# Kernel tuning notes

Hardware: AMD Instinct MI355X
Metric: run time of the kernel (lower is better)

## Reference

```python
import jax, jax.numpy as jnp
import numpy as np

# ---- constants mirroring the torch module ----
LOSS_ALPHA = 1.0      # args.loss_weight_alpha (intra-class weight)
LOSS_BETA = 1.0       # args.loss_weight_beta (focal weight)
FOCAL_GAMMA = 2.0
FOCAL_ALPHA = 0.85
EPS = 1e-09
LDAM_S = 30.0
CLS_NUM = np.array([85.0, 900.0])
LDAM_MAX_M = 0.5
LDAM_W = np.array([0.15, 0.85], dtype=np.float32)
B = 16777216


def setup_inputs() -> dict:
    key = jax.random.key(0)
    k1, k2 = jax.random.split(key)
    x = jax.random.uniform(k1, (B, 2), dtype=jnp.float32)  # [B, 2] probabilities-like logits
    target = jax.random.randint(k2, (B,), 0, 2)            # binary labels
    return {"x": x, "target": target}


def _intraclass_p(centered, std, target, cls):
    # correlation between consecutive same-class rows (sorted-index order),
    # vectorized: class-c indices first via stable argsort, mask invalid pairs.
    n_rows = centered.shape[0]
    mask = target == cls
    n = jnp.sum(mask)
    order = jnp.argsort(jnp.where(mask, jnp.arange(n_rows), n_rows))
    a, b = order[:-1], order[1:]
    corr = jnp.sum(centered[a] * centered[b], axis=1) / (std[a] * std[b])
    valid = jnp.arange(n_rows - 1) < (n - 1)
    s = jnp.sum(jnp.where(valid, corr, 0.0))
    return jnp.where(n > 0, s / jnp.maximum(n, 1).astype(s.dtype), 0.0)


def reference(x, target):
    num_cls = x.shape[1]
    # ---- LDAM loss ----
    m = 1.0 / np.sqrt(np.sqrt(CLS_NUM))
    m = m * (LDAM_MAX_M / np.max(m))
    m_list = jnp.asarray(m, jnp.float32)
    w = jnp.asarray(LDAM_W)
    batch_m = m_list[target]                                      # [B]
    onehot = jax.nn.one_hot(target, num_cls, dtype=bool)          # [B, C]
    out = jnp.where(onehot, x - batch_m[:, None], x)              # margin on target logit only
    logsm = jax.nn.log_softmax(LDAM_S * out, axis=-1)
    nll = -jnp.take_along_axis(logsm, target[:, None], axis=1)[:, 0]
    wi = w[target]
    ldam = jnp.sum(wi * nll) / jnp.sum(wi)                        # weighted-mean cross entropy
    # ---- binary focal loss (treats x[:,1] as probability) ----
    p = x[:, 1]
    t = target.astype(x.dtype)
    fl = (-FOCAL_ALPHA * t * (1.0 - p) ** FOCAL_GAMMA * jnp.log(p + EPS)
          - (1.0 - FOCAL_ALPHA) * (1.0 - t) * p ** FOCAL_GAMMA * jnp.log(1.0 - p + EPS))
    focal = jnp.mean(fl)
    # ---- intra-class correlation loss ----
    centered = x - jnp.mean(x, axis=1, keepdims=True)
    std = jnp.std(x, axis=1, ddof=1)                               # torch.std default: unbiased
    p0 = _intraclass_p(centered, std, target, 0)
    p1 = _intraclass_p(centered, std, target, 1)
    intra = (p0 - p1) ** 2
    return ldam + LOSS_BETA * focal + LOSS_ALPHA * intra
```

## Files before the change

kernel.cpp:

```cpp
#include <hip/hip_runtime.h>

#define E_BLOCK 8192
#define E_WAVE  2048
#define ITERS   16

#define M1      0.2771814156f
#define LDAM_S  30.0f

struct BlockRec {
  int s0, p0, s1, p1;
  float wnll, fl;
  int cnt1, pad;
};

__device__ __forceinline__ void comb0(int &s, int &f, int &l, int sb, int fb, int lb) {
  s += sb + l * fb;
  f = f ? f : fb;
  l = fb ? lb : l;
}

__device__ __forceinline__ void bfly_step(int m, int lane, int &s, int &f, int &l) {
  const int os = __shfl_xor(s, m), of = __shfl_xor(f, m), ol = __shfl_xor(l, m);
  const bool up = (lane & m) != 0;
  int as = up ? os : s, af = up ? of : f, al = up ? ol : l;
  const int bs = up ? s : os, bf = up ? f : of, bl = up ? l : ol;
  comb0(as, af, al, bs, bf, bl);
  s = as; f = af; l = al;
}

__global__ __launch_bounds__(256) void loss_pass1(
    const float* __restrict__ x, const int* __restrict__ tgt,
    BlockRec* __restrict__ recs, int B) {
  __shared__ unsigned int lds[3328];
  unsigned int* chunkw = lds;
  unsigned int* stw = lds + 2304;
  float* wnw = (float*)(lds + 2560);
  float* flw = (float*)(lds + 2816);
  int*   cnw = (int*)(lds + 3072);
  unsigned short* cs = (unsigned short*)lds;

  const int tid = threadIdx.x;
  const int w = tid >> 6, lane = tid & 63;
  const int waveBase = blockIdx.x * E_BLOCK + w * E_WAVE;

  float wnll = 0.f, fls = 0.f; int cnt1 = 0;

  for (int j = 0; j < ITERS; ++j) {
    const int e = waveBase + ((j << 6) + lane) * 2;
    unsigned int pk = 0;
    if (e < B) {
      const float4 xv = *reinterpret_cast<const float4*>(x + 2 * e);
      const int2  tv = *reinterpret_cast<const int2*>(tgt + e);
      unsigned int c[2];
      const float x0a = xv.x, x1a = xv.y; const float x0b = xv.z, x1b = xv.w;
      const int ta = tv.x, tb = tv.y;
      {
        const float d  = x0a - x1a;
        const float z  = LDAM_S * (ta ? (d + M1) : (0.5f - d));
        const float sp = fmaxf(z, 0.f) + __logf(1.f + __expf(-fabsf(z)));
        wnll += (ta ? 0.85f : 0.15f) * sp;
        const float p  = x1a;
        const float lg = __logf((ta ? p : (1.f - p)) + 1e-9f);
        const float cf = ta ? (-0.85f * (1.f - p) * (1.f - p)) : (-0.15f * p * p);
        fls += cf * lg;
        cnt1 += ta;
        c[0] = 4u | (unsigned)(x0a > x1a) | ((unsigned)ta << 1);
      }
      {
        const float d  = x0b - x1b;
        const float z  = LDAM_S * (tb ? (d + M1) : (0.5f - d));
        const float sp = fmaxf(z, 0.f) + __logf(1.f + __expf(-fabsf(z)));
        wnll += (tb ? 0.85f : 0.15f) * sp;
        const float p  = x1b;
        const float lg = __logf((tb ? p : (1.f - p)) + 1e-9f);
        const float cf = tb ? (-0.85f * (1.f - p) * (1.f - p)) : (-0.15f * p * p);
        fls += cf * lg;
        cnt1 += tb;
        c[1] = 4u | (unsigned)(x0b > x1b) | ((unsigned)tb << 1);
      }
      pk = c[0] | (c[1] << 8);
    }
    const int li2 = w * 1024 + (j << 6) + lane;
    cs[(li2 >> 4) * 18 + (li2 & 15)] = (unsigned short)pk;
  }
  __syncthreads();

  int s0 = 0, f0 = 0, l0 = 0, s1 = 0, f1 = 0, l1 = 0;
  #pragma unroll
  for (int r = 0; r < 8; ++r) {
    const unsigned int wv = chunkw[tid * 9 + r];
    #pragma unroll
    for (int k = 0; k < 4; ++k) {
      const unsigned int b = (wv >> (8 * k)) & 7u;
      if (b & 4u) {
        const int sv = (int)((b & 1u) << 1) - 1;
        const int t  = (int)((b >> 1) & 1u);
        const int lv = t ? l1 : l0;
        const int add = lv * sv;
        if (t) { s1 += add; l1 = sv; f1 = f1 ? f1 : sv; }
        else   { s0 += add; l0 = sv; f0 = f0 ? f0 : sv; }
      }
    }
  }
  stw[tid] = (unsigned)(s0 + 128) | ((unsigned)(f0 + 1) << 8) | ((unsigned)(l0 + 1) << 10)
           | ((unsigned)(s1 + 128) << 16) | ((unsigned)(f1 + 1) << 24) | ((unsigned)(l1 + 1) << 26);
  wnw[tid] = wnll; flw[tid] = fls; cnw[tid] = cnt1;
  __syncthreads();

  if (w == 0) {
    int S0 = 0, F0 = 0, L0 = 0, S1 = 0, F1 = 0, L1 = 0;
    float W = 0.f, F = 0.f; int C = 0;
    #pragma unroll
    for (int q = 0; q < 4; ++q) {
      const int i = lane * 4 + q;
      const unsigned int pk = stw[i];
      comb0(S0, F0, L0, (int)(pk & 255u) - 128, (int)((pk >> 8) & 3u) - 1, (int)((pk >> 10) & 3u) - 1);
      comb0(S1, F1, L1, (int)((pk >> 16) & 255u) - 128, (int)((pk >> 24) & 3u) - 1, (int)((pk >> 26) & 3u) - 1);
      W += wnw[i]; F += flw[i]; C += cnw[i];
    }
    #pragma unroll
    for (int k = 0; k < 6; ++k) {
      const int m = 1 << k;
      bfly_step(m, lane, S0, F0, L0);
      bfly_step(m, lane, S1, F1, L1);
      W += __shfl_xor(W, m); F += __shfl_xor(F, m); C += __shfl_xor(C, m);
    }
    if (lane == 0) {
      BlockRec r;
      r.s0 = S0; r.p0 = (F0 + 1) | ((L0 + 1) << 4);
      r.s1 = S1; r.p1 = (F1 + 1) | ((L1 + 1) << 4);
      r.wnll = W; r.fl = F; r.cnt1 = C; r.pad = 0;
      recs[blockIdx.x] = r;
    }
  }
}

__global__ __launch_bounds__(256) void loss_pass2(
    const BlockRec* __restrict__ recs, int NB, int B, float* __restrict__ out) {
  __shared__ int sS0[256], sF0[256], sL0[256], sS1[256], sF1[256], sL1[256], sC[256];
  __shared__ double sW[256], sFl[256];
  const int tid = threadIdx.x, w = tid >> 6, lane = tid & 63;
  const int R = (NB + 255) >> 8;

  int s0 = 0, f0 = 0, l0 = 0, s1 = 0, f1 = 0, l1 = 0;
  double W = 0.0, Fd = 0.0; int C = 0;
  for (int r = 0; r < R; ++r) {
    const int b = tid * R + r;
    if (b < NB) {
      const BlockRec rec = recs[b];
      comb0(s0, f0, l0, rec.s0, (rec.p0 & 3) - 1, ((rec.p0 >> 4) & 3) - 1);
      comb0(s1, f1, l1, rec.s1, (rec.p1 & 3) - 1, ((rec.p1 >> 4) & 3) - 1);
      W += (double)rec.wnll; Fd += (double)rec.fl; C += rec.cnt1;
    }
  }
  sS0[tid] = s0; sF0[tid] = f0; sL0[tid] = l0;
  sS1[tid] = s1; sF1[tid] = f1; sL1[tid] = l1;
  sC[tid] = C; sW[tid] = W; sFl[tid] = Fd;
  __syncthreads();

  if (w == 0) {
    int S0 = 0, F0 = 0, L0 = 0, S1 = 0, F1 = 0, L1 = 0; int Ct = 0;
    double Wt = 0.0, Ft = 0.0;
    #pragma unroll
    for (int q = 0; q < 4; ++q) {
      const int i = lane * 4 + q;
      comb0(S0, F0, L0, sS0[i], sF0[i], sL0[i]);
      comb0(S1, F1, L1, sS1[i], sF1[i], sL1[i]);
      Wt += sW[i]; Ft += sFl[i]; Ct += sC[i];
    }
    #pragma unroll
    for (int k = 0; k < 6; ++k) {
      const int m = 1 << k;
      bfly_step(m, lane, S0, F0, L0);
      bfly_step(m, lane, S1, F1, L1);
      Wt += __shfl_xor(Wt, m); Ft += __shfl_xor(Ft, m); Ct += __shfl_xor(Ct, m);
    }
    if (lane == 0) {
      const double n1 = (double)Ct, n0 = (double)B - n1;
      const double sw = 0.15 * n0 + 0.85 * n1;
      const double ldam  = Wt / sw;
      const double focal = Ft / (double)B;
      const double q0 = (n0 > 0.0) ? (double)S0 / n0 : 0.0;
      const double q1 = (n1 > 0.0) ? (double)S1 / n1 : 0.0;
      const double dq = q0 - q1;
      out[0] = (float)(ldam + focal + dq * dq);
    }
  }
}

extern "C" void kernel_launch(void* const* d_in, const int* in_sizes, int n_in,
                              void* d_out, int out_size, void* d_ws, size_t ws_size,
                              hipStream_t stream) {
  const float* x  = (const float*)d_in[0];
  const int* tgt  = (const int*)d_in[1];
  float* out      = (float*)d_out;
  const int B  = in_sizes[1];
  const int NB = (B + E_BLOCK - 1) / E_BLOCK;
  BlockRec* recs = (BlockRec*)d_ws;
  loss_pass1<<<NB, 256, 0, stream>>>(x, tgt, recs, B);
  loss_pass2<<<1, 256, 0, stream>>>(recs, NB, B, out);
}
```

Measured before the change: 245.0 us.

## Process four elements per lane with prefetched loads and branchless exp2/log2 math

Each lane now handles four consecutive elements per iteration using two float4 loads and one int4 target load. The next iteration's data is prefetched into registers before the current one is computed. The per-element math becomes branchless FMA form using the hardware exp2/log2 builtins, the ln2 scaling of the focal term is folded into one multiply at the end, and packed sign codes are written to shared memory as 32-bit words. A launch bound of 8 blocks per CU is added, which may constrain register allocation, and a separate scalar tail path covers partial waves.

```diff
diff --git a/kernel.cpp b/kernel.cpp
--- a/kernel.cpp
+++ b/kernel.cpp
@@ -2,10 +2,14 @@
 
 #define E_BLOCK 8192
 #define E_WAVE  2048
-#define ITERS   16
-
-#define M1      0.2771814156f
-#define LDAM_S  30.0f
+#define QITERS  8
+
+#define M1f     0.2771814156f
+#define C_A1    60.0f
+#define C_C1    (30.0f*M1f - 15.0f)
+
+#define EXP2F(v) __builtin_amdgcn_exp2f(v)
+#define LOG2F(v) __builtin_amdgcn_logf(v)
 
 struct BlockRec {
   int s0, p0, s1, p1;
@@ -28,7 +32,31 @@
   s = as; f = af; l = al;
 }
 
-__global__ __launch_bounds__(256) void loss_pass1(
+__device__ __forceinline__ void elem_math(float x0, float x1, int t, int k,
+                                          float &wnll, float &flraw, int &cnt1,
+                                          unsigned int &word) {
+  const float tf  = (float)t;
+  const float wgt = fmaf(tf, 0.7f, 0.15f);
+  const float d   = x0 - x1;
+  const float za  = fmaf(tf, C_A1, -30.0f);
+  const float zc  = fmaf(tf, C_C1, 15.0f);
+  const float z   = fmaf(za, d, zc);
+  const float ex  = EXP2F(fabsf(z) * -1.44269504f);
+  const float lp  = LOG2F(1.0f + ex);
+  const float sp  = fmaf(0.69314718f, lp, fmaxf(z, 0.0f));
+  wnll = fmaf(wgt, sp, wnll);
+  const float om  = 1.0f - x1;
+  const float q   = t ? x1 : om;
+  const float r   = t ? om : x1;
+  const float lg2 = LOG2F(q + 1e-9f);
+  const float wr2 = (wgt * r) * r;
+  flraw = fmaf(wr2, lg2, flraw);
+  cnt1 += t;
+  const unsigned int code = 4u | (unsigned int)(d > 0.0f) | ((unsigned int)t << 1);
+  word |= code << (8 * k);
+}
+
+__global__ __launch_bounds__(256, 8) void loss_pass1(
     const float* __restrict__ x, const int* __restrict__ tgt,
     BlockRec* __restrict__ recs, int B) {
   __shared__ unsigned int lds[3328];
@@ -37,51 +65,48 @@
   float* wnw = (float*)(lds + 2560);
   float* flw = (float*)(lds + 2816);
   int*   cnw = (int*)(lds + 3072);
-  unsigned short* cs = (unsigned short*)lds;
 
   const int tid = threadIdx.x;
   const int w = tid >> 6, lane = tid & 63;
   const int waveBase = blockIdx.x * E_BLOCK + w * E_WAVE;
 
-  float wnll = 0.f, fls = 0.f; int cnt1 = 0;
-
-  for (int j = 0; j < ITERS; ++j) {
-    const int e = waveBase + ((j << 6) + lane) * 2;
-    unsigned int pk = 0;
-    if (e < B) {
-      const float4 xv = *reinterpret_cast<const float4*>(x + 2 * e);
-      const int2  tv = *reinterpret_cast<const int2*>(tgt + e);
-      unsigned int c[2];
-      const float x0a = xv.x, x1a = xv.y; const float x0b = xv.z, x1b = xv.w;
-      const int ta = tv.x, tb = tv.y;
-      {
-        const float d  = x0a - x1a;
-        const float z  = LDAM_S * (ta ? (d + M1) : (0.5f - d));
-        const float sp = fmaxf(z, 0.f) + __logf(1.f + __expf(-fabsf(z)));
-        wnll += (ta ? 0.85f : 0.15f) * sp;
-        const float p  = x1a;
-        const float lg = __logf((ta ? p : (1.f - p)) + 1e-9f);
-        const float cf = ta ? (-0.85f * (1.f - p) * (1.f - p)) : (-0.15f * p * p);
-        fls += cf * lg;
-        cnt1 += ta;
-        c[0] = 4u | (unsigned)(x0a > x1a) | ((unsigned)ta << 1);
+  float wnll = 0.f, flraw = 0.f; int cnt1 = 0;
+
+  if (waveBase + E_WAVE <= B) {
+    const int e0 = waveBase + lane * 4;
+    const float4* __restrict__ px = (const float4*)(x + 2 * (size_t)e0);
+    const int4*   __restrict__ pt = (const int4*)(tgt + e0);
+
+    float4 xa = px[0], xb = px[1];
+    int4  t4 = pt[0];
+    for (int j = 0; j < QITERS; ++j) {
+      float4 xa_n, xb_n; int4 t4_n;
+      if (j + 1 < QITERS) {
+        const int o = (j + 1) * 128;
+        xa_n = px[o]; xb_n = px[o + 1]; t4_n = pt[(j + 1) * 64];
       }
-      {
-        const float d  = x0b - x1b;
-        const float z  = LDAM_S * (tb ? (d + M1) : (0.5f - d));
-        const float sp = fmaxf(z, 0.f) + __logf(1.f + __expf(-fabsf(z)));
-        wnll += (tb ? 0.85f : 0.15f) * sp;
-        const float p  = x1b;
-        const float lg = __logf((tb ? p : (1.f - p)) + 1e-9f);
-        const float cf = tb ? (-0.85f * (1.f - p) * (1.f - p)) : (-0.15f * p * p);
-        fls += cf * lg;
-        cnt1 += tb;
-        c[1] = 4u | (unsigned)(x0b > x1b) | ((unsigned)tb << 1);
+      unsigned int word = 0;
+      elem_math(xa.x, xa.y, t4.x, 0, wnll, flraw, cnt1, word);
+      elem_math(xa.z, xa.w, t4.y, 1, wnll, flraw, cnt1, word);
+      elem_math(xb.x, xb.y, t4.z, 2, wnll, flraw, cnt1, word);
+      elem_math(xb.z, xb.w, t4.w, 3, wnll, flraw, cnt1, word);
+      const int qi = w * 512 + (j << 6) + lane;
+      chunkw[(qi >> 3) * 9 + (qi & 7)] = word;
+      xa = xa_n; xb = xb_n; t4 = t4_n;
+    }
+  } else {
+    for (int j = 0; j < QITERS; ++j) {
+      unsigned int word = 0;
+      for (int k = 0; k < 4; ++k) {
+        const int e = waveBase + ((j << 6) + lane) * 4 + k;
+        if (e < B) {
+          elem_math(x[2 * (size_t)e], x[2 * (size_t)e + 1], tgt[e], k,
+                    wnll, flraw, cnt1, word);
+        }
       }
-      pk = c[0] | (c[1] << 8);
-    }
-    const int li2 = w * 1024 + (j << 6) + lane;
-    cs[(li2 >> 4) * 18 + (li2 & 15)] = (unsigned short)pk;
+      const int qi = w * 512 + (j << 6) + lane;
+      chunkw[(qi >> 3) * 9 + (qi & 7)] = word;
+    }
   }
   __syncthreads();
 
@@ -104,7 +129,7 @@
   }
   stw[tid] = (unsigned)(s0 + 128) | ((unsigned)(f0 + 1) << 8) | ((unsigned)(l0 + 1) << 10)
            | ((unsigned)(s1 + 128) << 16) | ((unsigned)(f1 + 1) << 24) | ((unsigned)(l1 + 1) << 26);
-  wnw[tid] = wnll; flw[tid] = fls; cnw[tid] = cnt1;
+  wnw[tid] = wnll; flw[tid] = flraw * -0.69314718f; cnw[tid] = cnt1;
   __syncthreads();
 
   if (w == 0) {
```

Measured after the change: 247.2 us. Within noise of the previous version (+0.9%).
